# Kernel optimization log

Hardware: AMD Instinct MI355X
Metric: run time of the kernel (lower is better)

The kernel has to match this reference:

```python
import jax, jax.numpy as jnp
import numpy as np

JACCARD_THRESH = 0.5
NEGPOS_RATIO = 3
V0, V1 = 0.1, 0.2  # SSD encoding variances


def setup_inputs() -> dict:
    key = jax.random.key(0)
    k1, k2, k3, k4, k5, k6, k7 = jax.random.split(key, 7)
    B, P, C, O = 128, 8732, 21, 16
    loc_data = jax.random.normal(k1, (B, P, 4), dtype=jnp.float32)
    conf_data = jax.random.normal(k2, (B, P, C), dtype=jnp.float32)
    # default boxes in center form (cx, cy, w, h), all in [0,1]
    cxcy = jax.random.uniform(k3, (P, 2), minval=0.05, maxval=0.95)
    wh = jax.random.uniform(k4, (P, 2), minval=0.05, maxval=0.6)
    dbox_list = jnp.concatenate([cxcy, wh], axis=1).astype(jnp.float32)
    # ground-truth boxes in corner form with guaranteed positive extent
    tl = jax.random.uniform(k5, (B, O, 2), minval=0.0, maxval=0.6)
    sz = jax.random.uniform(k6, (B, O, 2), minval=0.05, maxval=0.35)
    labels = jax.random.randint(k7, (B, O, 1), 0, C - 1).astype(jnp.float32)
    targets = jnp.concatenate([tl, tl + sz, labels], axis=2)
    return {"loc_data": loc_data, "conf_data": conf_data,
            "dbox_list": dbox_list, "targets": targets}


def _match_one(truths, labels, dbox):
    """SSD match for one image. truths:[O,4] corner, labels:[O], dbox:[P,4] center."""
    pf = jnp.concatenate([dbox[:, :2] - dbox[:, 2:] * 0.5,
                          dbox[:, :2] + dbox[:, 2:] * 0.5], axis=1)  # point form [P,4]
    lt = jnp.maximum(truths[:, None, :2], pf[None, :, :2])
    rb = jnp.minimum(truths[:, None, 2:], pf[None, :, 2:])
    whi = jnp.clip(rb - lt, 0.0)
    inter = whi[..., 0] * whi[..., 1]                                # [O,P]
    area_t = (truths[:, 2] - truths[:, 0]) * (truths[:, 3] - truths[:, 1])
    area_p = dbox[:, 2] * dbox[:, 3]
    ov = inter / (area_t[:, None] + area_p[None, :] - inter)         # jaccard [O,P]
    best_prior_idx = jnp.argmax(ov, axis=1)                          # [O]
    bto = jnp.max(ov, axis=0)                                        # [P]
    bti = jnp.argmax(ov, axis=0)                                     # [P]
    bto = bto.at[best_prior_idx].set(2.0)
    O = truths.shape[0]
    bti = jax.lax.fori_loop(0, O, lambda j, b: b.at[best_prior_idx[j]].set(j), bti)
    matched = truths[bti]                                            # [P,4]
    conf = labels[bti].astype(jnp.int32) + 1
    conf = jnp.where(bto < JACCARD_THRESH, 0, conf)
    g_cxcy = ((matched[:, :2] + matched[:, 2:]) * 0.5 - dbox[:, :2]) / (V0 * dbox[:, 2:])
    g_wh = jnp.log((matched[:, 2:] - matched[:, :2]) / dbox[:, 2:]) / V1
    return jnp.concatenate([g_cxcy, g_wh], axis=1), conf


def reference(loc_data, conf_data, dbox_list, targets):
    B, P, C = conf_data.shape
    loc_t, conf_t = jax.vmap(_match_one, in_axes=(0, 0, None))(
        targets[..., :4], targets[..., 4], dbox_list)
    pos = conf_t > 0                                                  # [B,P]
    # smooth L1 (beta=1), summed over positives
    ad = jnp.abs(loc_data - loc_t)
    sl1 = jnp.where(ad < 1.0, 0.5 * ad * ad, ad - 0.5)
    loss_l = jnp.sum(jnp.where(pos[..., None], sl1, 0.0))
    # per-prior cross entropy
    logp = jax.nn.log_softmax(conf_data, axis=-1)
    ce = -jnp.take_along_axis(logp, conf_t[..., None], axis=-1)[..., 0]  # [B,P]
    # hard negative mining via double argsort (rank in descending order)
    ce_neg = jnp.where(pos, 0.0, ce)
    loss_idx = jnp.argsort(-ce_neg, axis=1)
    idx_rank = jnp.argsort(loss_idx, axis=1)
    num_pos = jnp.sum(pos, axis=1, keepdims=True)
    num_neg = jnp.minimum(num_pos * NEGPOS_RATIO, P)
    neg = idx_rank < num_neg
    sel = pos | neg
    loss_c = jnp.sum(jnp.where(sel, ce, 0.0))
    N = jnp.sum(num_pos).astype(loc_data.dtype)
    return jnp.stack([loss_l / N, loss_c / N])
```

## Files before the change

### kernel.cpp

```cpp
#include <hip/hip_runtime.h>
#include <cstddef>

#define Bn 128
#define Pn 8732
#define Cn 21
#define On 16
#define MAGIC 0x13579BDFu

__device__ __forceinline__ void argmax_combine(float& v, int& p, float v2, int p2) {
  if (v2 > v || (v2 == v && p2 < p)) { v = v2; p = p2; }
}

__global__ __launch_bounds__(256) void stream_kernel(
    const float* __restrict__ conf, const float* __restrict__ dbox,
    const float* __restrict__ targets,
    float* __restrict__ ce0, unsigned char* __restrict__ pack,
    unsigned long long* __restrict__ keys) {
  const int wb = threadIdx.x >> 6, lane = threadIdx.x & 63;
  const int wave_g = blockIdx.x * 4 + wb;
  const int b = wave_g & 127;
  const int cg = wave_g >> 7;

  __shared__ float4 s_row4[4][336];
  __shared__ float s_tt[4][On * 5];
  __shared__ float s_ar[4][On];

  #pragma unroll
  for (int i = lane; i < On * 5; i += 64)
    s_tt[wb][i] = targets[(size_t)b * On * 5 + i];
  if (lane < On) {
    float x1 = targets[(size_t)b * On * 5 + lane * 5 + 0];
    float y1 = targets[(size_t)b * On * 5 + lane * 5 + 1];
    float x2 = targets[(size_t)b * On * 5 + lane * 5 + 2];
    float y2 = targets[(size_t)b * On * 5 + lane * 5 + 3];
    s_ar[wb][lane] = (x2 - x1) * (y2 - y1);
  }

  float bestv[On]; int bestp[On];
  #pragma unroll
  for (int j = 0; j < On; j++) { bestv[j] = -1.0f; bestp[j] = 0x7fffffff; }

  #pragma unroll
  for (int i = 0; i < 5; i++) {
    const int ci = cg + 32 * i;
    if (ci >= 137) break;
    const int p0 = ci * 64;
    const int rows = min(64, Pn - p0);
    const int n4 = rows * Cn / 4;

    const float4* src = (const float4*)(conf + ((size_t)b * Pn + p0) * Cn);
    float4 v0, v1, v2, v3, v4, v5;
    if (lane < n4)        v0 = src[lane];
    if (lane + 64 < n4)   v1 = src[lane + 64];
    if (lane + 128 < n4)  v2 = src[lane + 128];
    if (lane + 192 < n4)  v3 = src[lane + 192];
    if (lane + 256 < n4)  v4 = src[lane + 256];
    if (lane + 320 < n4)  v5 = src[lane + 320];
    if (lane < n4)        s_row4[wb][lane] = v0;
    if (lane + 64 < n4)   s_row4[wb][lane + 64] = v1;
    if (lane + 128 < n4)  s_row4[wb][lane + 128] = v2;
    if (lane + 192 < n4)  s_row4[wb][lane + 192] = v3;
    if (lane + 256 < n4)  s_row4[wb][lane + 256] = v4;
    if (lane + 320 < n4)  s_row4[wb][lane + 320] = v5;

    if (lane < rows) {
      const int p = p0 + lane;
      const float* x = (const float*)s_row4[wb] + lane * Cn;
      float m = x[0];
      #pragma unroll
      for (int q = 1; q < Cn; q++) m = fmaxf(m, x[q]);
      float s = 0.0f;
      #pragma unroll
      for (int q = 0; q < Cn; q++) s += expf(x[q] - m);
      float lse = m + logf(s);
      ce0[(size_t)b * Pn + p] = lse - x[0];

      float4 d = ((const float4*)dbox)[p];
      float px1 = d.x - d.z * 0.5f, py1 = d.y - d.w * 0.5f;
      float px2 = d.x + d.z * 0.5f, py2 = d.y + d.w * 0.5f;
      float ap = d.z * d.w;
      float mv = -1.0f; int mj = 0;
      #pragma unroll
      for (int j = 0; j < On; j++) {
        float lx = fmaxf(s_tt[wb][j*5+0], px1);
        float ly = fmaxf(s_tt[wb][j*5+1], py1);
        float rx = fminf(s_tt[wb][j*5+2], px2);
        float ry = fminf(s_tt[wb][j*5+3], py2);
        float w = fmaxf(rx - lx, 0.0f), h = fmaxf(ry - ly, 0.0f);
        float inter = w * h;
        float ov = inter / (s_ar[wb][j] + ap - inter);
        if (ov > bestv[j]) { bestv[j] = ov; bestp[j] = p; }
        if (ov > mv) { mv = ov; mj = j; }
      }
      pack[(size_t)b * Pn + p] =
          (unsigned char)(mj | ((mv >= 0.5f) ? 16 : 0));
    }
  }

  #pragma unroll
  for (int j = 0; j < On; j++) {
    float v = bestv[j]; int p = bestp[j];
    #pragma unroll
    for (int off = 32; off; off >>= 1) {
      float v2 = __shfl_down(v, off);
      int p2 = __shfl_down(p, off);
      argmax_combine(v, p, v2, p2);
    }
    if (lane == 0) {
      unsigned long long key;
      if (v < 0.0f) key = 0xC000000000000000ull;
      else key = (((unsigned long long)(__float_as_uint(v) | 0xC0000000u)) << 32)
               | (unsigned long long)(0xFFFFFFFFu - (unsigned)p);
      atomicMax(&keys[b * On + j], key);
    }
  }
}

__global__ __launch_bounds__(1024) void reduce_kernel(
    const float* __restrict__ loc, const float* __restrict__ conf,
    const float* __restrict__ dbox, const float* __restrict__ targets,
    const float* __restrict__ ce0, const unsigned char* __restrict__ pack,
    const unsigned long long* __restrict__ keys,
    unsigned int* __restrict__ res, float* __restrict__ out) {
  const int b = blockIdx.x;
  const int tid = threadIdx.x;
  const int wave = tid >> 6, lane = tid & 63;

  __shared__ float s_t[On * 5];
  __shared__ int s_bp[On];
  __shared__ unsigned hist[16][256];
  __shared__ float s_redf[2][16];
  __shared__ int s_redi[16];
  __shared__ unsigned s_prefix;
  __shared__ int s_kk;
  __shared__ int s_np;

  if (tid < On * 5) s_t[tid] = targets[(size_t)b * On * 5 + tid];
  if (tid < On)
    s_bp[tid] = (int)(0xFFFFFFFFu - (unsigned)(keys[b * On + tid] & 0xFFFFFFFFull));
  __syncthreads();

  float ce_r[9];
  float my_loc = 0.0f, my_cep = 0.0f; int my_np = 0;
  #pragma unroll
  for (int sI = 0; sI < 9; sI++) {
    ce_r[sI] = 0.0f;
    const int p = tid + 1024 * sI;
    if (p < Pn) {
      unsigned char pk = pack[(size_t)b * Pn + p];
      float c0 = ce0[(size_t)b * Pn + p];
      int pos = pk >> 4;
      int bt = pk & 15;
      #pragma unroll
      for (int j = 0; j < On; j++)
        if (s_bp[j] == p) { bt = j; pos = 1; }
      ce_r[sI] = pos ? 0.0f : c0;
      if (pos) {
        my_np++;
        const float* t = &s_t[bt * 5];
        int c = (int)t[4] + 1;
        const float* row = conf + ((size_t)b * Pn + p) * Cn;
        my_cep += c0 + row[0] - row[c];
        float4 d = ((const float4*)dbox)[p];
        float mx1 = t[0], my1 = t[1], mx2 = t[2], my2 = t[3];
        float g0 = ((mx1 + mx2) * 0.5f - d.x) / (0.1f * d.z);
        float g1 = ((my1 + my2) * 0.5f - d.y) / (0.1f * d.w);
        float g2 = logf((mx2 - mx1) / d.z) / 0.2f;
        float g3 = logf((my2 - my1) / d.w) / 0.2f;
        float4 ld = ((const float4*)loc)[(size_t)b * Pn + p];
        float g[4] = {g0, g1, g2, g3};
        float l[4] = {ld.x, ld.y, ld.z, ld.w};
        #pragma unroll
        for (int q = 0; q < 4; q++) {
          float ad = fabsf(l[q] - g[q]);
          my_loc += (ad < 1.0f) ? 0.5f * ad * ad : ad - 0.5f;
        }
      }
    }
  }

  {
    int np = my_np;
    #pragma unroll
    for (int off = 32; off; off >>= 1) np += __shfl_down(np, off);
    if (lane == 0) s_redi[wave] = np;
  }
  __syncthreads();
  if (tid == 0) {
    int np = 0;
    #pragma unroll
    for (int w = 0; w < 16; w++) np += s_redi[w];
    s_np = np;
  }
  __syncthreads();

  const int k = min(s_np * 3, Pn);
  unsigned prefix = 0, maskb = 0;
  int kk = k;
  for (int shift = 24; shift >= 0; shift -= 8) {
    #pragma unroll
    for (int j = 0; j < 4; j++) hist[wave][lane * 4 + j] = 0;
    __syncthreads();
    #pragma unroll
    for (int sI = 0; sI < 9; sI++) {
      const int p = tid + 1024 * sI;
      if (p < Pn) {
        unsigned u = __float_as_uint(ce_r[sI]);
        if ((u & maskb) == prefix) atomicAdd(&hist[wave][(u >> shift) & 255u], 1u);
      }
    }
    __syncthreads();
    if (tid < 256) {
      unsigned c = 0;
      #pragma unroll
      for (int w = 0; w < 16; w++) c += hist[w][tid];
      hist[0][tid] = c;
    }
    __syncthreads();
    if (tid == 0) {
      int cum = 0, chosen = 0;
      for (int bin = 255; bin >= 0; bin--) {
        int c = (int)hist[0][bin];
        if (cum + c >= kk) { chosen = bin; break; }
        cum += c;
      }
      s_prefix = prefix | ((unsigned)chosen << shift);
      s_kk = kk - cum;
    }
    __syncthreads();
    prefix = s_prefix; kk = s_kk;
    maskb |= 255u << shift;
    __syncthreads();
  }
  float T = __uint_as_float(prefix);

  float sum_gt = 0.0f; int cnt_gt = 0;
  #pragma unroll
  for (int sI = 0; sI < 9; sI++) {
    const int p = tid + 1024 * sI;
    if (p < Pn) {
      float x = ce_r[sI];
      if (x > T) { sum_gt += x; cnt_gt++; }
    }
  }
  #pragma unroll
  for (int off = 32; off; off >>= 1) {
    sum_gt += __shfl_down(sum_gt, off);
    cnt_gt += __shfl_down(cnt_gt, off);
    my_loc += __shfl_down(my_loc, off);
    my_cep += __shfl_down(my_cep, off);
  }
  if (lane == 0) {
    s_redf[0][wave] = my_loc; s_redf[1][wave] = sum_gt + my_cep; s_redi[wave] = cnt_gt;
  }
  __syncthreads();
  if (tid == 0) {
    float ll = 0.0f, lc = 0.0f; int cg = 0;
    #pragma unroll
    for (int w = 0; w < 16; w++) {
      ll += s_redf[0][w]; lc += s_redf[1][w]; cg += s_redi[w];
    }
    lc += (k > 0) ? (float)(k - cg) * T : 0.0f;
    atomicExch(&res[b * 4 + 0], __float_as_uint(ll));
    atomicExch(&res[b * 4 + 1], __float_as_uint(lc));
    atomicExch(&res[b * 4 + 2], (unsigned)s_np);
    __threadfence();
    atomicExch(&res[b * 4 + 3], MAGIC);
  }

  if (b == 0 && tid < 64) {
    float ll = 0.0f, lc = 0.0f; int np = 0;
    #pragma unroll
    for (int h = 0; h < 2; h++) {
      const int i = tid + 64 * h;
      while (atomicAdd(&res[i * 4 + 3], 0u) != MAGIC) { __builtin_amdgcn_s_sleep(8); }
      ll += __uint_as_float(atomicAdd(&res[i * 4 + 0], 0u));
      lc += __uint_as_float(atomicAdd(&res[i * 4 + 1], 0u));
      np += (int)atomicAdd(&res[i * 4 + 2], 0u);
    }
    #pragma unroll
    for (int off = 32; off; off >>= 1) {
      ll += __shfl_down(ll, off);
      lc += __shfl_down(lc, off);
      np += __shfl_down(np, off);
    }
    if (tid == 0) {
      float fN = (float)np;
      out[0] = ll / fN;
      out[1] = lc / fN;
    }
  }
}

extern "C" void kernel_launch(void* const* d_in, const int* in_sizes, int n_in,
                              void* d_out, int out_size, void* d_ws, size_t ws_size,
                              hipStream_t stream) {
  const float* loc_data  = (const float*)d_in[0];
  const float* conf_data = (const float*)d_in[1];
  const float* dbox      = (const float*)d_in[2];
  const float* targets   = (const float*)d_in[3];
  float* out = (float*)d_out;

  char* ws = (char*)d_ws;
  float* ce0 = (float*)ws;
  unsigned char* pack = (unsigned char*)(ws + (size_t)Bn * Pn * 4);
  unsigned long long* keys =
      (unsigned long long*)(ws + (size_t)Bn * Pn * 5);
  unsigned int* res = (unsigned int*)(ws + (size_t)Bn * Pn * 5 + Bn * On * 8);

  stream_kernel<<<1024, 256, 0, stream>>>(conf_data, dbox, targets, ce0, pack, keys);
  reduce_kernel<<<Bn, 1024, 0, stream>>>(loc_data, conf_data, dbox, targets,
                                         ce0, pack, keys, res, out);
}
```

Measured before the change: 234.4 us.

## Parallelize radix-select bin search and exit early via small candidate set

The radix top-k threshold search in the reduce kernel now finds the bin with a 64-lane wavefront prefix scan instead of a serial single-thread loop over 256 bins, which also removes one barrier per pass. The histogram is transposed to bin-major layout so each bin's per-wave counts are contiguous. Once the candidate bucket holds 64 or fewer values, the remaining radix passes are skipped: candidates are compacted into shared memory and ranked by brute-force comparison. This adds compaction atomics and more complex control flow, and correctness depends on the scan boundary conditions.

```diff
diff --git a/kernel.cpp b/kernel.cpp
--- a/kernel.cpp
+++ b/kernel.cpp
@@ -128,11 +128,15 @@
 
   __shared__ float s_t[On * 5];
   __shared__ int s_bp[On];
-  __shared__ unsigned hist[16][256];
+  __shared__ unsigned hist[256 * 16];
+  __shared__ unsigned s_col[256];
+  __shared__ unsigned s_cand[64];
   __shared__ float s_redf[2][16];
   __shared__ int s_redi[16];
   __shared__ unsigned s_prefix;
   __shared__ int s_kk;
+  __shared__ int s_cnt;
+  __shared__ int s_cc;
   __shared__ int s_np;
 
   if (tid < On * 5) s_t[tid] = targets[(size_t)b * On * 5 + tid];
@@ -197,40 +201,88 @@
   const int k = min(s_np * 3, Pn);
   unsigned prefix = 0, maskb = 0;
   int kk = k;
+  int cntc = Pn;
   for (int shift = 24; shift >= 0; shift -= 8) {
-    #pragma unroll
-    for (int j = 0; j < 4; j++) hist[wave][lane * 4 + j] = 0;
+    if (cntc <= 64) break;
+    ((uint4*)hist)[tid] = make_uint4(0u, 0u, 0u, 0u);
     __syncthreads();
     #pragma unroll
     for (int sI = 0; sI < 9; sI++) {
       const int p = tid + 1024 * sI;
       if (p < Pn) {
         unsigned u = __float_as_uint(ce_r[sI]);
-        if ((u & maskb) == prefix) atomicAdd(&hist[wave][(u >> shift) & 255u], 1u);
+        if ((u & maskb) == prefix)
+          atomicAdd(&hist[(((u >> shift) & 255u) << 4) + (unsigned)wave], 1u);
       }
     }
     __syncthreads();
     if (tid < 256) {
       unsigned c = 0;
       #pragma unroll
-      for (int w = 0; w < 16; w++) c += hist[w][tid];
-      hist[0][tid] = c;
-    }
-    __syncthreads();
-    if (tid == 0) {
-      int cum = 0, chosen = 0;
-      for (int bin = 255; bin >= 0; bin--) {
-        int c = (int)hist[0][bin];
-        if (cum + c >= kk) { chosen = bin; break; }
-        cum += c;
-      }
-      s_prefix = prefix | ((unsigned)chosen << shift);
-      s_kk = kk - cum;
-    }
-    __syncthreads();
-    prefix = s_prefix; kk = s_kk;
+      for (int w = 0; w < 16; w++) c += hist[(tid << 4) + w];
+      s_col[tid] = c;
+    }
+    __syncthreads();
+    if (tid < 64) {
+      unsigned c0 = s_col[4 * tid + 0], c1 = s_col[4 * tid + 1];
+      unsigned c2 = s_col[4 * tid + 2], c3 = s_col[4 * tid + 3];
+      unsigned t0 = c0 + c1 + c2 + c3;
+      unsigned S = t0;
+      #pragma unroll
+      for (int off = 1; off < 64; off <<= 1) {
+        unsigned o = __shfl_down(S, off);
+        if (tid + off < 64) S += o;
+      }
+      unsigned Snext = S - t0;
+      unsigned s3 = Snext + c3;
+      unsigned s2 = s3 + c2;
+      unsigned s1 = s2 + c1;
+      unsigned s0 = s1 + c0;
+      unsigned kk_u = (unsigned)kk;
+      int chosen = -1; unsigned snx = 0, cc = 0;
+      if (s3 >= kk_u && Snext < kk_u)      { chosen = 3; snx = Snext; cc = c3; }
+      else if (s2 >= kk_u && s3 < kk_u)    { chosen = 2; snx = s3;    cc = c2; }
+      else if (s1 >= kk_u && s2 < kk_u)    { chosen = 1; snx = s2;    cc = c1; }
+      else if (s0 >= kk_u && s1 < kk_u)    { chosen = 0; snx = s1;    cc = c0; }
+      if (chosen >= 0) {
+        s_prefix = prefix | ((unsigned)(4 * tid + chosen) << shift);
+        s_kk = (int)(kk_u - snx);
+        s_cnt = (int)cc;
+      }
+    }
+    __syncthreads();
+    prefix = s_prefix; kk = s_kk; cntc = s_cnt;
     maskb |= 255u << shift;
-    __syncthreads();
+  }
+  if (maskb != 0xFFFFFFFFu) {
+    if (tid == 0) s_cc = 0;
+    __syncthreads();
+    #pragma unroll
+    for (int sI = 0; sI < 9; sI++) {
+      const int p = tid + 1024 * sI;
+      if (p < Pn) {
+        unsigned u = __float_as_uint(ce_r[sI]);
+        if ((u & maskb) == prefix) {
+          int ix = atomicAdd(&s_cc, 1);
+          s_cand[ix] = u;
+        }
+      }
+    }
+    __syncthreads();
+    if (tid < 64) {
+      int c = s_cc;
+      if (tid < c) {
+        unsigned v = s_cand[tid];
+        int g = 0, e = 0;
+        for (int i = 0; i < c; i++) {
+          unsigned w = s_cand[i];
+          g += (w > v); e += (w == v);
+        }
+        if (g < kk && kk <= g + e) s_prefix = v;
+      }
+    }
+    __syncthreads();
+    prefix = s_prefix;
   }
   float T = __uint_as_float(prefix);
 
```

Measured after the change: 201.4 us. 1.16x faster.
